# Optimization experiments

Measured on AMD Instinct MI355X. Metric: run time of the kernel, lower is better.

The kernel has to match this reference:

```python
import jax, jax.numpy as jnp
import numpy as np

N_NODES = 100000
N_EDGES = 1600000
NODE_IN = 6
EDGE_IN = 4
HID = 128


def _glorot(key, shape):
    fan_in, fan_out = shape[0], shape[1]
    lim = (6.0 / (fan_in + fan_out)) ** 0.5
    return jax.random.uniform(key, shape, jnp.float32, -lim, lim)


def setup_inputs() -> dict:
    key = jax.random.key(0)
    ks = jax.random.split(key, 16)
    x = jax.random.normal(ks[0], (N_NODES, NODE_IN), jnp.float32)
    edge_index = jax.random.randint(ks[1], (2, N_EDGES), 0, N_NODES, jnp.int64)
    edge_attr = jax.random.normal(ks[2], (N_EDGES, EDGE_IN), jnp.float32)
    # SAGEConv params: out = x @ W_root + mean_neigh @ W_neigh + b
    params = {
        "w1_root": _glorot(ks[3], (NODE_IN, HID)),
        "w1_neigh": _glorot(ks[4], (NODE_IN, HID)),
        "b1": jnp.zeros((HID,), jnp.float32),
        "w2_root": _glorot(ks[5], (HID, HID)),
        "w2_neigh": _glorot(ks[6], (HID, HID)),
        "b2": jnp.zeros((HID,), jnp.float32),
        "w_e1": _glorot(ks[7], (2 * HID + EDGE_IN, HID)),
        "b_e1": jnp.zeros((HID,), jnp.float32),
        "w_e2": _glorot(ks[8], (HID, HID // 2)),
        "b_e2": jnp.zeros((HID // 2,), jnp.float32),
        "w_e3": _glorot(ks[9], (HID // 2, 1)),
        "b_e3": jnp.zeros((1,), jnp.float32),
    }
    return {"x": x, "edge_index": edge_index, "edge_attr": edge_attr, **params}


def _sage(x, src, dst, w_root, w_neigh, b):
    # mean aggregation of source features into destination nodes
    agg = jax.ops.segment_sum(x[src], dst, num_segments=N_NODES)
    cnt = jax.ops.segment_sum(jnp.ones((src.shape[0], 1), x.dtype), dst, num_segments=N_NODES)
    mean = agg / jnp.maximum(cnt, 1.0)
    return x @ w_root + mean @ w_neigh + b


def reference(x, edge_index, edge_attr,
              w1_root, w1_neigh, b1, w2_root, w2_neigh, b2,
              w_e1, b_e1, w_e2, b_e2, w_e3, b_e3):
    src, dst = edge_index[0], edge_index[1]
    h = jax.nn.relu(_sage(x, src, dst, w1_root, w1_neigh, b1))
    # dropout is identity in eval mode
    h = jax.nn.relu(_sage(h, src, dst, w2_root, w2_neigh, b2))
    # per-edge representation: [h[src], h[dst], edge_attr] -> MLP -> scalar
    e = jnp.concatenate([h[src], h[dst], edge_attr], axis=-1)  # [E, 2H+Ein]
    e = jax.nn.relu(e @ w_e1 + b_e1)
    e = jax.nn.relu(e @ w_e2 + b_e2)
    out = (e @ w_e3 + b_e3).squeeze(-1)  # [E]
    return out
```

## Files before the change

kernel.cpp:

```cpp
#include <hip/hip_runtime.h>
#include <hip/hip_bf16.h>
#include <stdint.h>


typedef unsigned short u16;
typedef short bf16x8 __attribute__((ext_vector_type(8)));
typedef float f32x4 __attribute__((ext_vector_type(4)));
typedef float f32x2 __attribute__((ext_vector_type(2)));

#define NMASK 0x1FFFF

__device__ __forceinline__ u16 f2b(float f) {
  unsigned u = __builtin_bit_cast(unsigned, f);
  u = u + 0x7fffu + ((u >> 16) & 1u);
  return (u16)(u >> 16);
}
__device__ __forceinline__ float bflo(unsigned u) {
  return __builtin_bit_cast(float, u << 16);
}
__device__ __forceinline__ float bfhi(unsigned u) {
  return __builtin_bit_cast(float, u & 0xffff0000u);
}
__device__ __forceinline__ f32x2 unpk2(unsigned u) {
  return (f32x2){bflo(u), bfhi(u)};
}
__device__ __forceinline__ unsigned pack2bf(float a, float b) {
  unsigned ua = __builtin_bit_cast(unsigned, a);
  unsigned ub = __builtin_bit_cast(unsigned, b);
  ua = ua + 0x7fffu + ((ua >> 16) & 1u);
  ub = ub + 0x7fffu + ((ub >> 16) & 1u);
  return (ua >> 16) | (ub & 0xffff0000u);
}

__global__ void hist_kernel(const int* __restrict__ ei, int* __restrict__ cnt,
                            int E) {
  int e = blockIdx.x * blockDim.x + threadIdx.x;
  if (e < E) atomicAdd(&cnt[ei[E + e]], 1);
}

__global__ void scan_block_sums(const int* __restrict__ cnt,
                                int* __restrict__ partial, int N) {
  __shared__ int red[256];
  int t = threadIdx.x;
  int n = blockIdx.x * 256 + t;
  red[t] = (n < N) ? cnt[n] : 0;
  __syncthreads();
  for (int off = 128; off; off >>= 1) {
    if (t < off) red[t] += red[t + off];
    __syncthreads();
  }
  if (t == 0) partial[blockIdx.x] = red[0];
}

__global__ void scan_partials(int* __restrict__ partial,
                              int* __restrict__ rowptr, int NBLK, int E,
                              int N) {
  __shared__ int sc[512];
  int t = threadIdx.x;
  int v = (t < NBLK) ? partial[t] : 0;
  sc[t] = v;
  __syncthreads();
  for (int off = 1; off < 512; off <<= 1) {
    int a = (t >= off) ? sc[t - off] : 0;
    __syncthreads();
    sc[t] += a;
    __syncthreads();
  }
  if (t < NBLK) partial[t] = sc[t] - v;
  if (t == 0) rowptr[N] = E;
}

__global__ void scan_final(const int* __restrict__ partial,
                           int* __restrict__ cursor, int* __restrict__ rowptr,
                           int N) {
  __shared__ int sc[256];
  int t = threadIdx.x;
  int n = blockIdx.x * 256 + t;
  int v = (n < N) ? cursor[n] : 0;
  sc[t] = v;
  __syncthreads();
  for (int off = 1; off < 256; off <<= 1) {
    int a = (t >= off) ? sc[t - off] : 0;
    __syncthreads();
    sc[t] += a;
    __syncthreads();
  }
  int excl = partial[blockIdx.x] + sc[t] - v;
  if (n < N) {
    rowptr[n] = excl;
    cursor[n] = excl;
  }
}

__global__ void scatter_csr(const int* __restrict__ ei,
                            const float* __restrict__ attr,
                            int* __restrict__ cursor, uint2* __restrict__ csr2,
                            float4* __restrict__ attrp, int E) {
  int e = blockIdx.x * blockDim.x + threadIdx.x;
  if (e >= E) return;
  int s = ei[e];
  int d = ei[E + e];
  float4 a4 = *(const float4*)(attr + (size_t)e * 4);
  int pos = atomicAdd(&cursor[d], 1);
  unsigned long long v = (unsigned long long)(unsigned)s |
                         ((unsigned long long)(unsigned)d << 17) |
                         ((unsigned long long)(unsigned)e << 34);
  csr2[pos] = make_uint2((unsigned)v, (unsigned)(v >> 32));
  attrp[pos] = a4;
}

__global__ void pack_weights(const float* __restrict__ w2_root,
                             const float* __restrict__ w2_neigh,
                             const float* __restrict__ w_e1,
                             const float* __restrict__ w_e2,
                             const float* __restrict__ b_e1,
                             u16* __restrict__ B2f, u16* __restrict__ WSDf,
                             u16* __restrict__ W2f, float* __restrict__ pbias) {
  int t = blockIdx.x * 256 + threadIdx.x;
  if (t < 32768) {
    int j = t & 7, lane = (t >> 3) & 63, nt = (t >> 9) & 7, kt = t >> 12;
    int k = kt * 32 + (lane >> 4) * 8 + j;
    int n = nt * 16 + (lane & 15);
    float v = (k < 128) ? w2_root[k * 128 + n] : w2_neigh[(k - 128) * 128 + n];
    B2f[t] = f2b(v);
  } else if (t < 65536) {
    int t2 = t - 32768;
    int j = t2 & 7, lane = (t2 >> 3) & 63, nt = (t2 >> 9) & 15, kt = t2 >> 13;
    int k = kt * 32 + (lane >> 4) * 8 + j;
    int n = nt * 16 + (lane & 15);
    float v = (n < 128) ? w_e1[k * 128 + n] : w_e1[(128 + k) * 128 + (n - 128)];
    WSDf[t2] = f2b(v);
  } else if (t < 73728) {
    int t2 = t - 65536;
    int j = t2 & 7, lane = (t2 >> 3) & 63, nt = (t2 >> 9) & 3, kt = t2 >> 11;
    int k = kt * 32 + (lane >> 4) * 8 + j;
    int n = nt * 16 + (lane & 15);
    W2f[t2] = f2b(w_e2[k * 64 + n]);
  } else if (t < 73984) {
    int n = t - 73728;
    pbias[n] = (n < 128) ? 0.0f : b_e1[n - 128];
  }
}

__global__ __launch_bounds__(256) void agg1_kernel(
    const float* __restrict__ x, const int* __restrict__ rowptr,
    const uint2* __restrict__ csr2, float* __restrict__ mean1, int N) {
  int n = blockIdx.x * 4 + (threadIdx.x >> 6);
  if (n >= N) return;
  int lane = threadIdx.x & 63;
  int g = lane >> 3;
  int c = lane & 7;
  int beg = rowptr[n], end = rowptr[n + 1];
  float a = 0.0f;
  if (c < 6) {
    for (int i = beg + g; i < end; i += 8) {
      int s = (int)(csr2[i].x & NMASK);
      a += x[(size_t)s * 6 + c];
    }
  }
  a += __shfl_xor(a, 8, 64);
  a += __shfl_xor(a, 16, 64);
  a += __shfl_xor(a, 32, 64);
  if (g == 0 && c < 6)
    mean1[(size_t)n * 6 + c] = a / (float)max(end - beg, 1);
}

__global__ void dense1_kernel(const float* __restrict__ x,
                              const float* __restrict__ mean1,
                              const float* __restrict__ w_root,
                              const float* __restrict__ w_neigh,
                              const float* __restrict__ b,
                              u16* __restrict__ cat2b, int N) {
  int n = blockIdx.x;
  int m = threadIdx.x;
  if (n >= N) return;
  float s = b[m];
#pragma unroll
  for (int j = 0; j < 6; j++) {
    s += x[(size_t)n * 6 + j] * w_root[j * 128 + m] +
         mean1[(size_t)n * 6 + j] * w_neigh[j * 128 + m];
  }
  cat2b[(size_t)n * 256 + m] = f2b(fmaxf(s, 0.0f));
}

__global__ __launch_bounds__(256) void agg2_kernel(
    const u16* __restrict__ cat2b, u16* __restrict__ cat2w,
    const int* __restrict__ rowptr, const uint2* __restrict__ csr2, int N) {
  int n = blockIdx.x * 4 + (threadIdx.x >> 6);
  if (n >= N) return;
  int lane = threadIdx.x & 63;
  int g = lane >> 4;
  int c = lane & 15;
  int beg = rowptr[n], end = rowptr[n + 1];
  f32x2 acc2[4];
#pragma unroll
  for (int j = 0; j < 4; j++) acc2[j] = (f32x2){0.f, 0.f};

  int i = beg + g;
  uint4 u0, u1;
  bool h0 = i < end, h1 = (i + 4) < end;
  if (h0)
    u0 = *(const uint4*)(cat2b + (size_t)(csr2[i].x & NMASK) * 256 + c * 8);
  if (h1)
    u1 = *(const uint4*)(cat2b + (size_t)(csr2[i + 4].x & NMASK) * 256 + c * 8);
  while (h0) {
    uint4 uc = u0;
    i += 4;
    h0 = h1;
    u0 = u1;
    h1 = (i + 4) < end;
    if (h1)
      u1 = *(const uint4*)(cat2b + (size_t)(csr2[i + 4].x & NMASK) * 256 + c * 8);
    acc2[0] += unpk2(uc.x);
    acc2[1] += unpk2(uc.y);
    acc2[2] += unpk2(uc.z);
    acc2[3] += unpk2(uc.w);
  }
#pragma unroll
  for (int j = 0; j < 4; j++) {
    acc2[j].x += __shfl_xor(acc2[j].x, 16, 64);
    acc2[j].y += __shfl_xor(acc2[j].y, 16, 64);
    acc2[j].x += __shfl_xor(acc2[j].x, 32, 64);
    acc2[j].y += __shfl_xor(acc2[j].y, 32, 64);
  }
  if (g == 0) {
    float inv = 1.0f / (float)max(end - beg, 1);
    uint4 ov;
    ov.x = pack2bf(acc2[0].x * inv, acc2[0].y * inv);
    ov.y = pack2bf(acc2[1].x * inv, acc2[1].y * inv);
    ov.z = pack2bf(acc2[2].x * inv, acc2[2].y * inv);
    ov.w = pack2bf(acc2[3].x * inv, acc2[3].y * inv);
    *(uint4*)(cat2w + (size_t)n * 256 + 128 + c * 8) = ov;
  }
}

template <int KT, int NT, bool RELU>
__global__ __launch_bounds__(256) void mfma_gemm(
    const u16* __restrict__ A, int lda, const u16* __restrict__ Bf,
    const float* __restrict__ bias, u16* __restrict__ C, int ldc, int M) {
  __shared__ u16 sB[KT * NT * 512];
  int tid = threadIdx.x;
  for (int i = tid; i < KT * NT * 64; i += 256)
    ((uint4*)sB)[i] = ((const uint4*)Bf)[i];
  int w = tid >> 6, l = tid & 63;
  int quad = l >> 4, col16 = l & 15;
  int rowA = blockIdx.x * 64 + w * 16 + col16;
  bool rv = rowA < M;
  const u16* ap = A + (size_t)rowA * lda + quad * 8;
  f32x4 acc[NT];
#pragma unroll
  for (int nt = 0; nt < NT; nt++) acc[nt] = (f32x4){0.f, 0.f, 0.f, 0.f};
  __syncthreads();
#pragma unroll
  for (int kt = 0; kt < KT; kt++) {
    bf16x8 av = {};
    if (rv) av = *(const bf16x8*)(ap + kt * 32);
#pragma unroll
    for (int nt = 0; nt < NT; nt++) {
      bf16x8 bv = *(const bf16x8*)(sB + ((kt * NT + nt) * 64 + l) * 8);
      acc[nt] = __builtin_amdgcn_mfma_f32_16x16x32_bf16(av, bv, acc[nt], 0, 0, 0);
    }
  }
  int rowbase = blockIdx.x * 64 + w * 16 + quad * 4;
#pragma unroll
  for (int r = 0; r < 4; r++) {
    int row = rowbase + r;
    if (row < M) {
#pragma unroll
      for (int nt = 0; nt < NT; nt++) {
        float v = acc[nt][r] + bias[nt * 16 + col16];
        if (RELU) v = fmaxf(v, 0.0f);
        C[(size_t)row * ldc + nt * 16 + col16] = f2b(v);
      }
    }
  }
}

__global__ __launch_bounds__(256) void edge_mfma_kernel(
    const u16* __restrict__ Pcatb, const uint2* __restrict__ csr2,
    const float4* __restrict__ attrp, const float* __restrict__ w_e1,
    const u16* __restrict__ W2f, const float* __restrict__ b_e2,
    const float* __restrict__ w_e3, const float* __restrict__ b_e3,
    float* __restrict__ out, int E) {
  __shared__ u16 sV[2][64 * 136];
  __shared__ u16 sW2[8192];

  int tid = threadIdx.x;
  int w = tid >> 6, l = tid & 63, quad = l >> 4, c16 = l & 15;
  int egrp = tid >> 4, ac16 = tid & 15;

  for (int i = tid; i < 1024; i += 256)
    ((uint4*)sW2)[i] = ((const uint4*)W2f)[i];

  f32x2 wa2[4][4];
#pragma unroll
  for (int j = 0; j < 4; j++) {
    float4 w0 = *(const float4*)(w_e1 + (256 + j) * 128 + ac16 * 8);
    float4 w1 = *(const float4*)(w_e1 + (256 + j) * 128 + ac16 * 8 + 4);
    wa2[j][0] = (f32x2){w0.x, w0.y};
    wa2[j][1] = (f32x2){w0.z, w0.w};
    wa2[j][2] = (f32x2){w1.x, w1.y};
    wa2[j][3] = (f32x2){w1.z, w1.w};
  }
  float w3v[4], be2[4];
#pragma unroll
  for (int nt = 0; nt < 4; nt++) {
    w3v[nt] = w_e3[nt * 16 + c16];
    be2[nt] = b_e2[nt * 16 + c16];
  }
  float b3 = b_e3[0];

  int tiles = (E + 63) >> 6;
  int S = gridDim.x;

  uint2 pk[4];
  uint4 ps[4], pd[4];
  float4 at[4];
  int eidr[4];

  auto load_pk = [&](int t) {
#pragma unroll
    for (int it = 0; it < 4; it++) {
      int e = min(t * 64 + it * 16 + egrp, E - 1);
      pk[it] = csr2[e];
    }
  };
  auto issue_gather = [&](int t) {
#pragma unroll
    for (int it = 0; it < 4; it++) {
      unsigned long long v = ((unsigned long long)pk[it].y << 32) | pk[it].x;
      int s = (int)(v & NMASK);
      int d = (int)((v >> 17) & NMASK);
      eidr[it] = (int)(v >> 34);
      ps[it] = *(const uint4*)(Pcatb + (size_t)s * 256 + ac16 * 8);
      pd[it] = *(const uint4*)(Pcatb + (size_t)d * 256 + 128 + ac16 * 8);
      int e = min(t * 64 + it * 16 + egrp, E - 1);
      at[it] = attrp[e];
    }
  };

  int t = blockIdx.x;
  if (t < tiles) {
    load_pk(t);
    issue_gather(t);
    if (t + S < tiles) load_pk(t + S);
  }
  int buf = 0;
  for (; t < tiles; t += S) {
    u16* sv = sV[buf];
#pragma unroll
    for (int it = 0; it < 4; it++) {
      int e = it * 16 + egrp;
      uint4 psu = ps[it], pdu = pd[it];
      float4 a4 = at[it];
      unsigned pu[4] = {psu.x, psu.y, psu.z, psu.w};
      unsigned du[4] = {pdu.x, pdu.y, pdu.z, pdu.w};
      uint4 ov;
      unsigned* op = (unsigned*)&ov;
#pragma unroll
      for (int p2 = 0; p2 < 4; p2++) {
        f32x2 f = unpk2(pu[p2]) + unpk2(du[p2]);
        f += a4.x * wa2[0][p2];
        f += a4.y * wa2[1][p2];
        f += a4.z * wa2[2][p2];
        f += a4.w * wa2[3][p2];
        f = __builtin_elementwise_max(f, (f32x2){0.f, 0.f});
        op[p2] = pack2bf(f.x, f.y);
      }
      *(uint4*)(sv + e * 136 + ac16 * 8) = ov;
      if (ac16 == 0) *(unsigned*)(sv + e * 136 + 128) = (unsigned)eidr[it];
    }
    if (t + S < tiles) {
      issue_gather(t + S);
      if (t + 2 * S < tiles) load_pk(t + 2 * S);
    }
    __syncthreads();
    f32x4 acc[4];
#pragma unroll
    for (int nt = 0; nt < 4; nt++) acc[nt] = (f32x4){0.f, 0.f, 0.f, 0.f};
    const u16* vp = sV[buf] + (w * 16 + c16) * 136 + quad * 8;
#pragma unroll
    for (int kt = 0; kt < 4; kt++) {
      bf16x8 av = *(const bf16x8*)(vp + kt * 32);
#pragma unroll
      for (int nt = 0; nt < 4; nt++) {
        bf16x8 bv = *(const bf16x8*)(sW2 + ((kt * 4 + nt) * 64 + l) * 8);
        acc[nt] = __builtin_amdgcn_mfma_f32_16x16x32_bf16(av, bv, acc[nt], 0, 0, 0);
      }
    }
#pragma unroll
    for (int r = 0; r < 4; r++) {
      float p = 0.0f;
#pragma unroll
      for (int nt = 0; nt < 4; nt++)
        p += fmaxf(acc[nt][r] + be2[nt], 0.0f) * w3v[nt];
      p += __shfl_xor(p, 1, 64);
      p += __shfl_xor(p, 2, 64);
      p += __shfl_xor(p, 4, 64);
      p += __shfl_xor(p, 8, 64);
      if (c16 == 0) {
        int eloc = w * 16 + quad * 4 + r;
        if (t * 64 + eloc < E) {
          unsigned eid = *(const unsigned*)(sV[buf] + eloc * 136 + 128);
          out[eid] = p + b3;
        }
      }
    }
    buf ^= 1;
  }
}

extern "C" void kernel_launch(void* const* d_in, const int* in_sizes, int n_in,
                              void* d_out, int out_size, void* d_ws,
                              size_t ws_size, hipStream_t stream) {
  const float* x        = (const float*)d_in[0];
  const int*   ei       = (const int*)d_in[1];
  const float* attr     = (const float*)d_in[2];
  const float* w1_root  = (const float*)d_in[3];
  const float* w1_neigh = (const float*)d_in[4];
  const float* b1       = (const float*)d_in[5];
  const float* w2_root  = (const float*)d_in[6];
  const float* w2_neigh = (const float*)d_in[7];
  const float* b2       = (const float*)d_in[8];
  const float* w_e1     = (const float*)d_in[9];
  const float* b_e1     = (const float*)d_in[10];
  const float* w_e2     = (const float*)d_in[11];
  const float* b_e2     = (const float*)d_in[12];
  const float* w_e3     = (const float*)d_in[13];
  const float* b_e3     = (const float*)d_in[14];
  float* out = (float*)d_out;

  int N = in_sizes[0] / 6;
  int E = in_sizes[2] / 4;
  int NBLK = (N + 255) / 256;

  int* wsi = (int*)d_ws;
  int*    rowptr  = wsi;
  int*    cursor  = wsi + 100004;
  int*    partial = wsi + 200004;
  uint2*  csr2    = (uint2*)(wsi + 200520);
  float*  mean1   = (float*)(wsi + 3400520);
  u16*    cat2b   = (u16*)(wsi + 4000520);
  u16*    h2b     = (u16*)(wsi + 16800520);
  u16*    B2f     = (u16*)(wsi + 23200520);
  u16*    WSDf    = (u16*)(wsi + 23216904);
  u16*    W2f     = (u16*)(wsi + 23233288);
  float*  pbias   = (float*)(wsi + 23237384);
  float4* attrp   = (float4*)(wsi + 23237640);

  hipMemsetAsync(cursor, 0, (size_t)N * sizeof(int), stream);

  pack_weights<<<289, 256, 0, stream>>>(w2_root, w2_neigh, w_e1, w_e2, b_e1,
                                        B2f, WSDf, W2f, pbias);

  hist_kernel<<<(E + 255) / 256, 256, 0, stream>>>(ei, cursor, E);
  scan_block_sums<<<NBLK, 256, 0, stream>>>(cursor, partial, N);
  scan_partials<<<1, 512, 0, stream>>>(partial, rowptr, NBLK, E, N);
  scan_final<<<NBLK, 256, 0, stream>>>(partial, cursor, rowptr, N);
  scatter_csr<<<(E + 255) / 256, 256, 0, stream>>>(ei, attr, cursor, csr2,
                                                   attrp, E);

  agg1_kernel<<<(N + 3) / 4, 256, 0, stream>>>(x, rowptr, csr2, mean1, N);
  dense1_kernel<<<N, 128, 0, stream>>>(x, mean1, w1_root, w1_neigh, b1, cat2b, N);

  agg2_kernel<<<(N + 3) / 4, 256, 0, stream>>>(cat2b, cat2b, rowptr, csr2, N);

  int gblocks = (N + 63) / 64;
  mfma_gemm<8, 8, true><<<gblocks, 256, 0, stream>>>(cat2b, 256, B2f, b2, h2b,
                                                     128, N);
  mfma_gemm<4, 16, false><<<gblocks, 256, 0, stream>>>(h2b, 128, WSDf, pbias,
                                                       cat2b, 256, N);

  edge_mfma_kernel<<<1024, 256, 0, stream>>>(cat2b, csr2, attrp, w_e1, W2f,
                                             b_e2, w_e3, b_e3, out, E);
}
```

Before: 612.0 us.

## Batch gather loads in aggregation kernels, restructure dense1, single-buffer edge LDS

The agg1 and agg2 kernels now load several neighbour indices and their feature rows up front, so more gathers are in flight before accumulation starts, with a scalar tail loop for high-degree nodes. dense1 becomes a persistent grid-stride kernel that keeps weights in registers and stages x and mean1 rows for 32 nodes in shared memory, instead of launching one block per node. The edge kernel drops its double-buffered LDS tile in favour of one buffer plus a __syncthreads per tile, which cuts LDS use but adds a barrier. Bf16 packing switches to the HIP intrinsic for round-to-nearest conversion.

```diff
diff --git a/kernel.cpp b/kernel.cpp
--- a/kernel.cpp
+++ b/kernel.cpp
@@ -30,6 +30,12 @@
   ua = ua + 0x7fffu + ((ua >> 16) & 1u);
   ub = ub + 0x7fffu + ((ub >> 16) & 1u);
   return (ua >> 16) | (ub & 0xffff0000u);
+}
+__device__ __forceinline__ unsigned packrn(f32x2 f) {
+  __hip_bfloat162 h = __float22bfloat162_rn(make_float2(f.x, f.y));
+  unsigned r;
+  __builtin_memcpy(&r, &h, 4);
+  return r;
 }
 
 __global__ void hist_kernel(const int* __restrict__ ei, int* __restrict__ cnt,
@@ -153,8 +159,21 @@
   int beg = rowptr[n], end = rowptr[n + 1];
   float a = 0.0f;
   if (c < 6) {
-    for (int i = beg + g; i < end; i += 8) {
-      int s = (int)(csr2[i].x & NMASK);
+    int idx[4];
+#pragma unroll
+    for (int j = 0; j < 4; j++) {
+      int ii = beg + g + j * 8;
+      idx[j] = (ii < end) ? (int)(csr2[ii].x & NMASK) : -1;
+    }
+    float v[4];
+#pragma unroll
+    for (int j = 0; j < 4; j++)
+      v[j] = x[(size_t)(idx[j] < 0 ? 0 : idx[j]) * 6 + c];
+#pragma unroll
+    for (int j = 0; j < 4; j++)
+      if (idx[j] >= 0) a += v[j];
+    for (int ii = beg + g + 32; ii < end; ii += 8) {
+      int s = (int)(csr2[ii].x & NMASK);
       a += x[(size_t)s * 6 + c];
     }
   }
@@ -165,22 +184,44 @@
     mean1[(size_t)n * 6 + c] = a / (float)max(end - beg, 1);
 }
 
-__global__ void dense1_kernel(const float* __restrict__ x,
-                              const float* __restrict__ mean1,
-                              const float* __restrict__ w_root,
-                              const float* __restrict__ w_neigh,
-                              const float* __restrict__ b,
-                              u16* __restrict__ cat2b, int N) {
-  int n = blockIdx.x;
-  int m = threadIdx.x;
-  if (n >= N) return;
-  float s = b[m];
+__global__ __launch_bounds__(256) void dense1_kernel(
+    const float* __restrict__ x, const float* __restrict__ mean1,
+    const float* __restrict__ w_root, const float* __restrict__ w_neigh,
+    const float* __restrict__ b, u16* __restrict__ cat2b, int N) {
+  __shared__ float sxm[384];
+  int t = threadIdx.x;
+  int col = t & 127;
+  int half = t >> 7;
+  float wr[6], wn[6];
 #pragma unroll
   for (int j = 0; j < 6; j++) {
-    s += x[(size_t)n * 6 + j] * w_root[j * 128 + m] +
-         mean1[(size_t)n * 6 + j] * w_neigh[j * 128 + m];
-  }
-  cat2b[(size_t)n * 256 + m] = f2b(fmaxf(s, 0.0f));
+    wr[j] = w_root[j * 128 + col];
+    wn[j] = w_neigh[j * 128 + col];
+  }
+  float bb = b[col];
+  for (int base = blockIdx.x * 32; base < N; base += gridDim.x * 32) {
+    int cnt = min(32, N - base) * 6;
+    __syncthreads();
+    for (int i = t; i < 384; i += 256) {
+      if (i < 192)
+        sxm[i] = (i < cnt) ? x[(size_t)base * 6 + i] : 0.0f;
+      else
+        sxm[i] = (i - 192 < cnt) ? mean1[(size_t)base * 6 + (i - 192)] : 0.0f;
+    }
+    __syncthreads();
+#pragma unroll
+    for (int sub = 0; sub < 16; sub++) {
+      int nl = sub * 2 + half;
+      int n = base + nl;
+      if (n < N) {
+        float s = bb;
+#pragma unroll
+        for (int j = 0; j < 6; j++)
+          s += sxm[nl * 6 + j] * wr[j] + sxm[192 + nl * 6 + j] * wn[j];
+        cat2b[(size_t)n * 256 + col] = f2b(fmaxf(s, 0.0f));
+      }
+    }
+  }
 }
 
 __global__ __launch_bounds__(256) void agg2_kernel(
@@ -196,25 +237,35 @@
 #pragma unroll
   for (int j = 0; j < 4; j++) acc2[j] = (f32x2){0.f, 0.f};
 
-  int i = beg + g;
-  uint4 u0, u1;
-  bool h0 = i < end, h1 = (i + 4) < end;
-  if (h0)
-    u0 = *(const uint4*)(cat2b + (size_t)(csr2[i].x & NMASK) * 256 + c * 8);
-  if (h1)
-    u1 = *(const uint4*)(cat2b + (size_t)(csr2[i + 4].x & NMASK) * 256 + c * 8);
-  while (h0) {
-    uint4 uc = u0;
-    i += 4;
-    h0 = h1;
-    u0 = u1;
-    h1 = (i + 4) < end;
-    if (h1)
-      u1 = *(const uint4*)(cat2b + (size_t)(csr2[i + 4].x & NMASK) * 256 + c * 8);
-    acc2[0] += unpk2(uc.x);
-    acc2[1] += unpk2(uc.y);
-    acc2[2] += unpk2(uc.z);
-    acc2[3] += unpk2(uc.w);
+  const int DEPTH = 6;
+  int idx[DEPTH];
+#pragma unroll
+  for (int j = 0; j < DEPTH; j++) {
+    int ii = beg + g + j * 4;
+    idx[j] = (ii < end) ? (int)(csr2[ii].x & NMASK) : -1;
+  }
+  uint4 u[DEPTH];
+#pragma unroll
+  for (int j = 0; j < DEPTH; j++) {
+    int s = idx[j] < 0 ? 0 : idx[j];
+    u[j] = *(const uint4*)(cat2b + (size_t)s * 256 + c * 8);
+  }
+#pragma unroll
+  for (int j = 0; j < DEPTH; j++) {
+    if (idx[j] >= 0) {
+      acc2[0] += unpk2(u[j].x);
+      acc2[1] += unpk2(u[j].y);
+      acc2[2] += unpk2(u[j].z);
+      acc2[3] += unpk2(u[j].w);
+    }
+  }
+  for (int ii = beg + g + DEPTH * 4; ii < end; ii += 4) {
+    int s = (int)(csr2[ii].x & NMASK);
+    uint4 uu = *(const uint4*)(cat2b + (size_t)s * 256 + c * 8);
+    acc2[0] += unpk2(uu.x);
+    acc2[1] += unpk2(uu.y);
+    acc2[2] += unpk2(uu.z);
+    acc2[3] += unpk2(uu.w);
   }
 #pragma unroll
   for (int j = 0; j < 4; j++) {
@@ -226,10 +277,10 @@
   if (g == 0) {
     float inv = 1.0f / (float)max(end - beg, 1);
     uint4 ov;
-    ov.x = pack2bf(acc2[0].x * inv, acc2[0].y * inv);
-    ov.y = pack2bf(acc2[1].x * inv, acc2[1].y * inv);
-    ov.z = pack2bf(acc2[2].x * inv, acc2[2].y * inv);
-    ov.w = pack2bf(acc2[3].x * inv, acc2[3].y * inv);
+    ov.x = packrn(acc2[0] * inv);
+    ov.y = packrn(acc2[1] * inv);
+    ov.z = packrn(acc2[2] * inv);
+    ov.w = packrn(acc2[3] * inv);
     *(uint4*)(cat2w + (size_t)n * 256 + 128 + c * 8) = ov;
   }
 }
@@ -282,7 +333,7 @@
     const u16* __restrict__ W2f, const float* __restrict__ b_e2,
     const float* __restrict__ w_e3, const float* __restrict__ b_e3,
     float* __restrict__ out, int E) {
-  __shared__ u16 sV[2][64 * 136];
+  __shared__ u16 sV[64 * 136];
   __shared__ u16 sW2[8192];
 
   int tid = threadIdx.x;
@@ -345,9 +396,7 @@
     issue_gather(t);
     if (t + S < tiles) load_pk(t + S);
   }
-  int buf = 0;
   for (; t < tiles; t += S) {
-    u16* sv = sV[buf];
 #pragma unroll
     for (int it = 0; it < 4; it++) {
       int e = it * 16 + egrp;
@@ -365,10 +414,10 @@
         f += a4.z * wa2[2][p2];
         f += a4.w * wa2[3][p2];
         f = __builtin_elementwise_max(f, (f32x2){0.f, 0.f});
-        op[p2] = pack2bf(f.x, f.y);
+        op[p2] = packrn(f);
       }
-      *(uint4*)(sv + e * 136 + ac16 * 8) = ov;
-      if (ac16 == 0) *(unsigned*)(sv + e * 136 + 128) = (unsigned)eidr[it];
+      *(uint4*)(sV + e * 136 + ac16 * 8) = ov;
+      if (ac16 == 0) *(unsigned*)(sV + e * 136 + 128) = (unsigned)eidr[it];
     }
     if (t + S < tiles) {
       issue_gather(t + S);
@@ -378,7 +427,7 @@
     f32x4 acc[4];
 #pragma unroll
     for (int nt = 0; nt < 4; nt++) acc[nt] = (f32x4){0.f, 0.f, 0.f, 0.f};
-    const u16* vp = sV[buf] + (w * 16 + c16) * 136 + quad * 8;
+    const u16* vp = sV + (w * 16 + c16) * 136 + quad * 8;
 #pragma unroll
     for (int kt = 0; kt < 4; kt++) {
       bf16x8 av = *(const bf16x8*)(vp + kt * 32);
@@ -401,12 +450,12 @@
       if (c16 == 0) {
         int eloc = w * 16 + quad * 4 + r;
         if (t * 64 + eloc < E) {
-          unsigned eid = *(const unsigned*)(sV[buf] + eloc * 136 + 128);
+          unsigned eid = *(const unsigned*)(sV + eloc * 136 + 128);
           out[eid] = p + b3;
         }
       }
     }
-    buf ^= 1;
+    __syncthreads();
   }
 }
 
@@ -448,7 +497,7 @@
   float*  pbias   = (float*)(wsi + 23237384);
   float4* attrp   = (float4*)(wsi + 23237640);
 
-  hipMemsetAsync(cursor, 0, (size_t)N * sizeof(int), stream);
+  (void)hipMemsetAsync(cursor, 0, (size_t)N * sizeof(int), stream);
 
   pack_weights<<<289, 256, 0, stream>>>(w2_root, w2_neigh, w_e1, w_e2, b_e1,
                                         B2f, WSDf, W2f, pbias);
@@ -461,7 +510,8 @@
                                                    attrp, E);
 
   agg1_kernel<<<(N + 3) / 4, 256, 0, stream>>>(x, rowptr, csr2, mean1, N);
-  dense1_kernel<<<N, 128, 0, stream>>>(x, mean1, w1_root, w1_neigh, b1, cat2b, N);
+  dense1_kernel<<<1024, 256, 0, stream>>>(x, mean1, w1_root, w1_neigh, b1,
+                                          cat2b, N);
 
   agg2_kernel<<<(N + 3) / 4, 256, 0, stream>>>(cat2b, cat2b, rowptr, csr2, N);
 
```

Measured after the change: 604.0 us. No clear change (-1.3%).
